# Performance work log

Hardware: AMD Instinct MI355X
Metric: run time of the kernel (lower is better)

## Reference

```python
import jax, jax.numpy as jnp
import numpy as np

EPS = 1e-5
NUM_GN_GROUPS = 32


def setup_inputs() -> dict:
    key = jax.random.key(0)
    k1, k2, k3 = jax.random.split(key, 3)
    B, C, N, G = 2, 256, 4096, 8
    c = C // G
    return {
        "points": jax.random.normal(k1, (B, C, N), dtype=jnp.float32),
        "conv_w": jax.random.normal(k2, (G, c, c), dtype=jnp.float32) / np.sqrt(c),
        "conv_b": jax.random.normal(k3, (C,), dtype=jnp.float32) * 0.02,
        "gn_w": jnp.ones((C,), dtype=jnp.float32),
        "gn_b": jnp.zeros((C,), dtype=jnp.float32),
    }


def reference(points, conv_w, conv_b, gn_w, gn_b):
    B, C, N = points.shape
    G = conv_w.shape[0]
    c = C // G  # channels per attention group
    identity = points

    # grouped 1x1 conv: per-group [c,c] matmul + bias
    x = points.reshape(B, G, c, N)
    x = jnp.einsum('gij,bgjn->bgin', conv_w, x) + conv_b.reshape(1, G, c, 1)

    # attention[b,g,n,m] = sum_i x[b,g,i,n] * x[b,g,i,m] / sqrt(c)
    scale = 1.0 / np.sqrt(c).astype(np.float32)
    attn = jnp.einsum('bgin,bgim->bgnm', x, x) * scale
    # softmax over dim=2 (the query/row N axis -- non-standard)
    attn = jax.nn.softmax(attn, axis=2)

    # ELU-gated second matmul: [B,G,c,N] @ [B,G,N,N] -> [B,G,c,N]
    x = jnp.einsum('bgcn,bgnm->bgcm', jax.nn.elu(x), attn)

    # channel shuffle: [B,G,c,N] -> [B,c,G,N] -> [B,C,N]
    x = x.transpose(0, 2, 1, 3).reshape(B, C, N)
    x = x + identity

    # GroupNorm(32 groups) over (channels-in-group, N)
    xg = x.reshape(B, NUM_GN_GROUPS, C // NUM_GN_GROUPS, N)
    mean = xg.mean(axis=(2, 3), keepdims=True)
    var = xg.var(axis=(2, 3), keepdims=True)
    xg = (xg - mean) * jax.lax.rsqrt(var + EPS)
    x = xg.reshape(B, C, N)
    return x * gn_w.reshape(1, C, 1) + gn_b.reshape(1, C, 1)
```

## Files before the change

kernel.cpp:

```cpp
#include <hip/hip_runtime.h>

typedef __attribute__((ext_vector_type(8))) short bf16x8;
typedef __attribute__((ext_vector_type(4))) short bf16x4;
typedef __attribute__((ext_vector_type(4))) float f32x4;

#if __has_builtin(__builtin_amdgcn_exp2f)
#define EXP2(x) __builtin_amdgcn_exp2f(x)
#else
#define EXP2(x) exp2f(x)
#endif

__device__ __forceinline__ unsigned short f2bf(float f) {
    union { float f; unsigned int u; } v; v.f = f;
    unsigned int r = v.u + 0x7fffu + ((v.u >> 16) & 1u);
    return (unsigned short)(r >> 16);
}

__device__ __forceinline__ float asf(unsigned int u) {
    union { unsigned int u; float f; } v; v.u = u; return v.f;
}

#define QK_PRESCALE 0.50500983f

__global__ __launch_bounds__(256) void conv_kernel(
    const float* __restrict__ points, const float* __restrict__ conv_w,
    const float* __restrict__ conv_b,
    unsigned short* __restrict__ xqT, unsigned short* __restrict__ xv)
{
    __shared__ float w[1024];
    const int h  = blockIdx.x >> 6;
    const int nc = blockIdx.x & 63;
    const int g  = h & 7;
    const int tid = threadIdx.x;
    const float* wg = conv_w + g * 1024;
    for (int k = tid; k < 1024; k += 256) w[k] = wg[k];
    __syncthreads();
    const int n  = nc * 64 + (tid & 63);
    const int ig = tid >> 6;
    const float* p = points + (size_t)h * 32 * 4096 + n;
    float pv[32];
#pragma unroll
    for (int j = 0; j < 32; ++j) pv[j] = p[(size_t)j * 4096];
    float out[8];
#pragma unroll
    for (int ii = 0; ii < 8; ++ii) {
        const int i = ig * 8 + ii;
        float acc = conv_b[g * 32 + i];
        const float4* w4 = (const float4*)(w + i * 32);
#pragma unroll
        for (int j4 = 0; j4 < 8; ++j4) {
            float4 ww = w4[j4];
            acc += ww.x * pv[j4 * 4]     + ww.y * pv[j4 * 4 + 1]
                 + ww.z * pv[j4 * 4 + 2] + ww.w * pv[j4 * 4 + 3];
        }
        out[ii] = acc;
    }
    unsigned short tq[8];
#pragma unroll
    for (int ii = 0; ii < 8; ++ii) tq[ii] = f2bf(out[ii] * QK_PRESCALE);
    *(bf16x8*)(xqT + ((size_t)h * 4096 + n) * 32 + ig * 8) = *(bf16x8*)tq;
#pragma unroll
    for (int ii = 0; ii < 8; ++ii) {
        float x = out[ii];
        float e = x > 0.f ? x : (__expf(x) - 1.f);
        xv[((size_t)h * 32 + ig * 8 + ii) * 4096 + n] = f2bf(e);
    }
}

#define VSTR 136
#define PSTR 72

#if __has_builtin(__builtin_amdgcn_cvt_pk_bf16_f32)
typedef __attribute__((ext_vector_type(2))) __bf16 bf16x2v;
__device__ __forceinline__ bf16x4 exp_pack(f32x4 sc, float& lsum) {
    float e0 = EXP2(sc[0]), e1 = EXP2(sc[1]);
    float e2 = EXP2(sc[2]), e3 = EXP2(sc[3]);
    lsum += (e0 + e1) + (e2 + e3);
    union { bf16x2v v[2]; bf16x4 s; } u;
    u.v[0] = __builtin_amdgcn_cvt_pk_bf16_f32(e0, e1);
    u.v[1] = __builtin_amdgcn_cvt_pk_bf16_f32(e2, e3);
    return u.s;
}
#else
__device__ __forceinline__ bf16x4 exp_pack(f32x4 sc, float& lsum) {
    union { float f; unsigned int u; } e0, e1, e2, e3;
    e0.f = EXP2(sc[0]); e1.f = EXP2(sc[1]); e2.f = EXP2(sc[2]); e3.f = EXP2(sc[3]);
    unsigned int t0 = e0.u & 0xffff0000u, t1 = e1.u & 0xffff0000u;
    unsigned int t2 = e2.u & 0xffff0000u, t3 = e3.u & 0xffff0000u;
    lsum += (asf(t0) + asf(t1)) + (asf(t2) + asf(t3));
    union { unsigned int d[2]; bf16x4 v; } pk;
    pk.d[0] = (t0 >> 16) | t1;
    pk.d[1] = (t2 >> 16) | t3;
    return pk.v;
}
#endif

#define CHUNK(C0, KU, KP, VCUR, VNXT)                                          \
    {                                                                          \
        __syncthreads();                                                       \
        *(bf16x8*)((VNXT) + vi * VSTR + vn)      = va;                         \
        *(bf16x8*)((VNXT) + vi * VSTR + vn + 64) = vb;                         \
        const int pf1 = ((C0) + 128) & 4095;                                   \
        const int pf2 = ((C0) + 256) & 4095;                                   \
        va = *(const bf16x8*)(vbase + (size_t)vi * 4096 + pf2 + vn);           \
        vb = *(const bf16x8*)(vbase + (size_t)vi * 4096 + pf2 + vn + 64);      \
        _Pragma("unroll")                                                      \
        for (int s8 = 0; s8 < 8; ++s8)                                         \
            KP[s8] = *(const bf16x8*)(kfp + (size_t)(pf1 + s8 * 16) * 32);     \
        _Pragma("unroll")                                                      \
        for (int sub = 0; sub < 2; ++sub) {                                    \
            _Pragma("unroll")                                                  \
            for (int s = 0; s < 4; ++s) {                                      \
                f32x4 sc = __builtin_amdgcn_mfma_f32_16x16x32_bf16(            \
                    KU[sub * 4 + s], qfrag, (f32x4){0.f, 0.f, 0.f, 0.f},       \
                    0, 0, 0);                                                  \
                bf16x4 pk = exp_pack(sc, lsum);                                \
                *(bf16x4*)(pw + l15 * PSTR + s * 16 + quad * 4) = pk;          \
            }                                                                  \
            _Pragma("unroll")                                                  \
            for (int ng = 0; ng < 2; ++ng) {                                   \
                bf16x8 pfrag = *(const bf16x8*)(pw + l15 * PSTR + ng * 32 +    \
                                                quad * 8);                     \
                const int col = sub * 64 + ng * 32 + quad * 8;                 \
                bf16x8 v0 = *(const bf16x8*)((VCUR) + l15 * VSTR + col);       \
                bf16x8 v1 = *(const bf16x8*)((VCUR) + (16 + l15) * VSTR + col);\
                acc0 = __builtin_amdgcn_mfma_f32_16x16x32_bf16(v0, pfrag,      \
                                                               acc0, 0, 0, 0); \
                acc1 = __builtin_amdgcn_mfma_f32_16x16x32_bf16(v1, pfrag,      \
                                                               acc1, 0, 0, 0); \
            }                                                                  \
        }                                                                      \
    }

__global__ __launch_bounds__(256, 4) void attn_kernel(
    const unsigned short* __restrict__ xqT,
    const unsigned short* __restrict__ xv,
    const float* __restrict__ points,
    float* __restrict__ z, float* __restrict__ pstats)
{
    __shared__ unsigned short Vt0[32 * VSTR];
    __shared__ unsigned short Vt1[32 * VSTR];
    __shared__ unsigned short Pl[4][16 * PSTR];

    const int bid = blockIdx.x;
    const int h  = (bid & 7) * 2 + ((bid >> 3) & 1);
    const int qt = bid >> 4;
    const int b = h >> 3, g = h & 7;
    const int tid = threadIdx.x;
    const int wv = tid >> 6, lane = tid & 63;
    const int quad = lane >> 4, l15 = lane & 15;

    const int m = qt * 64 + wv * 16 + l15;

    const unsigned short* kbase = xqT + (size_t)h * 4096 * 32;
    const unsigned short* vbase = xv  + (size_t)h * 32 * 4096;

    const bf16x8 qfrag = *(const bf16x8*)(kbase + (size_t)m * 32 + quad * 8);

    f32x4 acc0 = {0.f, 0.f, 0.f, 0.f};
    f32x4 acc1 = {0.f, 0.f, 0.f, 0.f};
    float lsum = 0.f;

    const int vi = tid >> 3, vn = (tid & 7) * 8;
    unsigned short* pw = &Pl[wv][0];

    const unsigned short* kfp = kbase + (size_t)l15 * 32 + quad * 8;

    {
        bf16x8 t0 = *(const bf16x8*)(vbase + (size_t)vi * 4096 + vn);
        bf16x8 t1 = *(const bf16x8*)(vbase + (size_t)vi * 4096 + vn + 64);
        *(bf16x8*)(Vt0 + vi * VSTR + vn)      = t0;
        *(bf16x8*)(Vt0 + vi * VSTR + vn + 64) = t1;
    }
    bf16x8 va = *(const bf16x8*)(vbase + (size_t)vi * 4096 + 128 + vn);
    bf16x8 vb = *(const bf16x8*)(vbase + (size_t)vi * 4096 + 128 + vn + 64);
    bf16x8 kA[8], kB[8];
#pragma unroll
    for (int s8 = 0; s8 < 8; ++s8)
        kA[s8] = *(const bf16x8*)(kfp + (size_t)(s8 * 16) * 32);

    for (int n0 = 0; n0 < 4096; n0 += 256) {
        CHUNK(n0,       kA, kB, Vt0, Vt1);
        CHUNK(n0 + 128, kB, kA, Vt1, Vt0);
    }

    lsum += __shfl_xor(lsum, 16, 64);
    lsum += __shfl_xor(lsum, 32, 64);
    const float inv = 1.f / lsum;

    const float* pb = points + (size_t)b * 256 * 4096;
    float* zb = z + (size_t)b * 256 * 4096;
    float* sb = pstats + ((size_t)bid * 4 + wv) * 64;

#pragma unroll
    for (int half = 0; half < 2; ++half) {
        f32x4 a = half ? acc1 : acc0;
#pragma unroll
        for (int r = 0; r < 4; ++r) {
            const int i = half * 16 + quad * 4 + r;
            const size_t off = (size_t)(i * 8 + g) * 4096;
            float zA = a[r] * inv + pb[off + m];
            zb[off + m] = zA;
            float s  = zA;
            float ss = zA * zA;
            s += __shfl_xor(s, 1, 64);  ss += __shfl_xor(ss, 1, 64);
            s += __shfl_xor(s, 2, 64);  ss += __shfl_xor(ss, 2, 64);
            s += __shfl_xor(s, 4, 64);  ss += __shfl_xor(ss, 4, 64);
            s += __shfl_xor(s, 8, 64);  ss += __shfl_xor(ss, 8, 64);
            if (l15 == 0) {
                sb[i * 2]     = s;
                sb[i * 2 + 1] = ss;
            }
        }
    }
}

__global__ __launch_bounds__(256) void gn_combine(const float* __restrict__ pstats,
                                                  float* __restrict__ stats)
{
    const int b = blockIdx.x >> 5;
    const int i = blockIdx.x & 31;
    const int tid = threadIdx.x;
    float s = 0.f, ss = 0.f;
    for (int k = tid; k < 2048; k += 256) {
        const int wvk = k & 3, j = k >> 2;
        const int bid = (j & 3) | (b << 2) | ((j >> 2) << 3);
        const float* p = pstats + ((size_t)bid * 4 + wvk) * 64 + i * 2;
        s += p[0]; ss += p[1];
    }
#pragma unroll
    for (int off = 32; off > 0; off >>= 1) {
        s  += __shfl_down(s, off, 64);
        ss += __shfl_down(ss, off, 64);
    }
    __shared__ float red[8];
    const int w = tid >> 6;
    if ((tid & 63) == 0) { red[w * 2] = s; red[w * 2 + 1] = ss; }
    __syncthreads();
    if (tid == 0) {
        s  = red[0] + red[2] + red[4] + red[6];
        ss = red[1] + red[3] + red[5] + red[7];
        float mean = s * (1.f / 32768.f);
        float var  = ss * (1.f / 32768.f) - mean * mean;
        stats[blockIdx.x * 2]     = mean;
        stats[blockIdx.x * 2 + 1] = rsqrtf(var + 1e-5f);
    }
}

__global__ __launch_bounds__(256) void gn_apply(float* __restrict__ z,
                                                const float* __restrict__ stats,
                                                const float* __restrict__ gw,
                                                const float* __restrict__ gb)
{
    const int idx = blockIdx.x * 256 + threadIdx.x;
    float4* p = (float4*)z;
    float4 v = p[idx];
    const int chg = idx >> 10;
    const int blk = chg >> 3;
    const int ch  = chg & 255;
    const float mean = stats[blk * 2], rstd = stats[blk * 2 + 1];
    const float w  = gw[ch] * rstd;
    const float bb = gb[ch] - mean * w;
    v.x = v.x * w + bb; v.y = v.y * w + bb;
    v.z = v.z * w + bb; v.w = v.w * w + bb;
    p[idx] = v;
}

extern "C" void kernel_launch(void* const* d_in, const int* in_sizes, int n_in,
                              void* d_out, int out_size, void* d_ws, size_t ws_size,
                              hipStream_t stream)
{
    const float* points = (const float*)d_in[0];
    const float* conv_w = (const float*)d_in[1];
    const float* conv_b = (const float*)d_in[2];
    const float* gn_w   = (const float*)d_in[3];
    const float* gn_b   = (const float*)d_in[4];
    float* out = (float*)d_out;
    char* ws = (char*)d_ws;
    unsigned short* xqT = (unsigned short*)ws;
    unsigned short* xv  = (unsigned short*)(ws + (size_t)4 * 1024 * 1024);
    float* pstats = (float*)(ws + (size_t)8 * 1024 * 1024);
    float* stats  = (float*)(ws + (size_t)9 * 1024 * 1024);

    conv_kernel<<<1024, 256, 0, stream>>>(points, conv_w, conv_b, xqT, xv);
    attn_kernel<<<1024, 256, 0, stream>>>(xqT, xv, points, out, pstats);
    gn_combine<<<64, 256, 0, stream>>>(pstats, stats);
    gn_apply<<<2048, 256, 0, stream>>>(out, stats, gn_w, gn_b);
}
```

Baseline: 158.0 us.

## Split attention key range in two halves with separate combine kernel

The attention kernel now splits the 4096-long key dimension into two halves, doubling the grid to 2048 blocks. Each block writes unnormalized partial outputs and partial softmax sums to workspace, and a new combine kernel merges them, adds the residual and emits GroupNorm partial stats. The V tile goes from double buffering to a single shared buffer with an extra barrier. This aims for more parallelism and occupancy, at the cost of partial-result traffic, an extra launch and more synchronization per chunk.

```diff
diff --git a/kernel.cpp b/kernel.cpp
--- a/kernel.cpp
+++ b/kernel.cpp
@@ -95,18 +95,18 @@
 }
 #endif
 
-#define CHUNK(C0, KU, KP, VCUR, VNXT)                                          \
+#define CHUNK(C0, KU, KP)                                                      \
     {                                                                          \
         __syncthreads();                                                       \
-        *(bf16x8*)((VNXT) + vi * VSTR + vn)      = va;                         \
-        *(bf16x8*)((VNXT) + vi * VSTR + vn + 64) = vb;                         \
-        const int pf1 = ((C0) + 128) & 4095;                                   \
-        const int pf2 = ((C0) + 256) & 4095;                                   \
-        va = *(const bf16x8*)(vbase + (size_t)vi * 4096 + pf2 + vn);           \
-        vb = *(const bf16x8*)(vbase + (size_t)vi * 4096 + pf2 + vn + 64);      \
+        *(bf16x8*)(Vt + vi * VSTR + vn)      = va;                             \
+        *(bf16x8*)(Vt + vi * VSTR + vn + 64) = vb;                             \
+        __syncthreads();                                                       \
+        const int pfb = ((C0) + 128) & 2047;                                   \
+        va = *(const bf16x8*)(vbaseh + (size_t)vi * 4096 + pfb + vn);          \
+        vb = *(const bf16x8*)(vbaseh + (size_t)vi * 4096 + pfb + vn + 64);     \
         _Pragma("unroll")                                                      \
         for (int s8 = 0; s8 < 8; ++s8)                                         \
-            KP[s8] = *(const bf16x8*)(kfp + (size_t)(pf1 + s8 * 16) * 32);     \
+            KP[s8] = *(const bf16x8*)(kfph + (size_t)(pfb + s8 * 16) * 32);    \
         _Pragma("unroll")                                                      \
         for (int sub = 0; sub < 2; ++sub) {                                    \
             _Pragma("unroll")                                                  \
@@ -122,8 +122,8 @@
                 bf16x8 pfrag = *(const bf16x8*)(pw + l15 * PSTR + ng * 32 +    \
                                                 quad * 8);                     \
                 const int col = sub * 64 + ng * 32 + quad * 8;                 \
-                bf16x8 v0 = *(const bf16x8*)((VCUR) + l15 * VSTR + col);       \
-                bf16x8 v1 = *(const bf16x8*)((VCUR) + (16 + l15) * VSTR + col);\
+                bf16x8 v0 = *(const bf16x8*)(Vt + l15 * VSTR + col);           \
+                bf16x8 v1 = *(const bf16x8*)(Vt + (16 + l15) * VSTR + col);    \
                 acc0 = __builtin_amdgcn_mfma_f32_16x16x32_bf16(v0, pfrag,      \
                                                                acc0, 0, 0, 0); \
                 acc1 = __builtin_amdgcn_mfma_f32_16x16x32_bf16(v1, pfrag,      \
@@ -135,17 +135,18 @@
 __global__ __launch_bounds__(256, 4) void attn_kernel(
     const unsigned short* __restrict__ xqT,
     const unsigned short* __restrict__ xv,
-    const float* __restrict__ points,
-    float* __restrict__ z, float* __restrict__ pstats)
-{
-    __shared__ unsigned short Vt0[32 * VSTR];
-    __shared__ unsigned short Vt1[32 * VSTR];
+    float* __restrict__ opart, float* __restrict__ lpart)
+{
+    __shared__ unsigned short Vt[32 * VSTR];
     __shared__ unsigned short Pl[4][16 * PSTR];
 
     const int bid = blockIdx.x;
-    const int h  = (bid & 7) * 2 + ((bid >> 3) & 1);
-    const int qt = bid >> 4;
-    const int b = h >> 3, g = h & 7;
+    const int x  = bid & 7;
+    const int r  = bid >> 3;
+    const int h  = x * 2 + (r & 1);
+    const int rr = r >> 1;
+    const int qt = rr & 63;
+    const int kh = rr >> 6;
     const int tid = threadIdx.x;
     const int wv = tid >> 6, lane = tid & 63;
     const int quad = lane >> 4, l15 = lane & 15;
@@ -153,7 +154,7 @@
     const int m = qt * 64 + wv * 16 + l15;
 
     const unsigned short* kbase = xqT + (size_t)h * 4096 * 32;
-    const unsigned short* vbase = xv  + (size_t)h * 32 * 4096;
+    const unsigned short* vbaseh = xv + (size_t)h * 32 * 4096 + kh * 2048;
 
     const bf16x8 qfrag = *(const bf16x8*)(kbase + (size_t)m * 32 + quad * 8);
 
@@ -164,54 +165,75 @@
     const int vi = tid >> 3, vn = (tid & 7) * 8;
     unsigned short* pw = &Pl[wv][0];
 
-    const unsigned short* kfp = kbase + (size_t)l15 * 32 + quad * 8;
-
-    {
-        bf16x8 t0 = *(const bf16x8*)(vbase + (size_t)vi * 4096 + vn);
-        bf16x8 t1 = *(const bf16x8*)(vbase + (size_t)vi * 4096 + vn + 64);
-        *(bf16x8*)(Vt0 + vi * VSTR + vn)      = t0;
-        *(bf16x8*)(Vt0 + vi * VSTR + vn + 64) = t1;
-    }
-    bf16x8 va = *(const bf16x8*)(vbase + (size_t)vi * 4096 + 128 + vn);
-    bf16x8 vb = *(const bf16x8*)(vbase + (size_t)vi * 4096 + 128 + vn + 64);
+    const unsigned short* kfph =
+        kbase + ((size_t)kh * 2048 + l15) * 32 + quad * 8;
+
+    bf16x8 va = *(const bf16x8*)(vbaseh + (size_t)vi * 4096 + vn);
+    bf16x8 vb = *(const bf16x8*)(vbaseh + (size_t)vi * 4096 + vn + 64);
     bf16x8 kA[8], kB[8];
 #pragma unroll
     for (int s8 = 0; s8 < 8; ++s8)
-        kA[s8] = *(const bf16x8*)(kfp + (size_t)(s8 * 16) * 32);
-
-    for (int n0 = 0; n0 < 4096; n0 += 256) {
-        CHUNK(n0,       kA, kB, Vt0, Vt1);
-        CHUNK(n0 + 128, kB, kA, Vt1, Vt0);
+        kA[s8] = *(const bf16x8*)(kfph + (size_t)(s8 * 16) * 32);
+
+    for (int n0 = 0; n0 < 2048; n0 += 256) {
+        CHUNK(n0,       kA, kB);
+        CHUNK(n0 + 128, kB, kA);
     }
 
     lsum += __shfl_xor(lsum, 16, 64);
     lsum += __shfl_xor(lsum, 32, 64);
-    const float inv = 1.f / lsum;
-
+
+    const int ml = wv * 16 + l15;
+    const size_t hq2 = ((size_t)h * 64 + qt) * 2 + kh;
+    float* ob = opart + hq2 * 2048;
+#pragma unroll
+    for (int half = 0; half < 2; ++half) {
+        f32x4 a = half ? acc1 : acc0;
+#pragma unroll
+        for (int rr2 = 0; rr2 < 4; ++rr2) {
+            const int i = half * 16 + quad * 4 + rr2;
+            ob[i * 64 + ml] = a[rr2];
+        }
+    }
+    if (quad == 0) lpart[hq2 * 64 + ml] = lsum;
+}
+
+__global__ __launch_bounds__(256) void combine_kernel(
+    const float* __restrict__ opart, const float* __restrict__ lpart,
+    const float* __restrict__ points, float* __restrict__ z,
+    float* __restrict__ pstats)
+{
+    const int bid2 = blockIdx.x;
+    const int h = bid2 >> 6, qt = bid2 & 63;
+    const int b = h >> 3, g = h & 7;
+    const int tid = threadIdx.x;
+    const int w = tid >> 6, lane = tid & 63;
+    const int mg = qt * 64 + lane;
+
+    const float la = lpart[(size_t)(bid2 * 2) * 64 + lane];
+    const float lb = lpart[(size_t)(bid2 * 2 + 1) * 64 + lane];
+    const float inv = 1.f / (la + lb);
+
+    const float* oa = opart + (size_t)(bid2 * 2) * 2048;
+    const float* obp = opart + (size_t)(bid2 * 2 + 1) * 2048;
     const float* pb = points + (size_t)b * 256 * 4096;
     float* zb = z + (size_t)b * 256 * 4096;
-    float* sb = pstats + ((size_t)bid * 4 + wv) * 64;
-
-#pragma unroll
-    for (int half = 0; half < 2; ++half) {
-        f32x4 a = half ? acc1 : acc0;
-#pragma unroll
-        for (int r = 0; r < 4; ++r) {
-            const int i = half * 16 + quad * 4 + r;
-            const size_t off = (size_t)(i * 8 + g) * 4096;
-            float zA = a[r] * inv + pb[off + m];
-            zb[off + m] = zA;
-            float s  = zA;
-            float ss = zA * zA;
-            s += __shfl_xor(s, 1, 64);  ss += __shfl_xor(ss, 1, 64);
-            s += __shfl_xor(s, 2, 64);  ss += __shfl_xor(ss, 2, 64);
-            s += __shfl_xor(s, 4, 64);  ss += __shfl_xor(ss, 4, 64);
-            s += __shfl_xor(s, 8, 64);  ss += __shfl_xor(ss, 8, 64);
-            if (l15 == 0) {
-                sb[i * 2]     = s;
-                sb[i * 2 + 1] = ss;
-            }
-        }
+    float* sb = pstats + (size_t)bid2 * 64;
+
+#pragma unroll
+    for (int ii = 0; ii < 8; ++ii) {
+        const int i = w * 8 + ii;
+        const size_t off = (size_t)(i * 8 + g) * 4096 + mg;
+        float v = (oa[i * 64 + lane] + obp[i * 64 + lane]) * inv + pb[off];
+        zb[off] = v;
+        float s = v, ss = v * v;
+        s += __shfl_xor(s, 1, 64);   ss += __shfl_xor(ss, 1, 64);
+        s += __shfl_xor(s, 2, 64);   ss += __shfl_xor(ss, 2, 64);
+        s += __shfl_xor(s, 4, 64);   ss += __shfl_xor(ss, 4, 64);
+        s += __shfl_xor(s, 8, 64);   ss += __shfl_xor(ss, 8, 64);
+        s += __shfl_xor(s, 16, 64);  ss += __shfl_xor(ss, 16, 64);
+        s += __shfl_xor(s, 32, 64);  ss += __shfl_xor(ss, 32, 64);
+        if (lane == 0) { sb[i * 2] = s; sb[i * 2 + 1] = ss; }
     }
 }
 
@@ -222,10 +244,8 @@
     const int i = blockIdx.x & 31;
     const int tid = threadIdx.x;
     float s = 0.f, ss = 0.f;
-    for (int k = tid; k < 2048; k += 256) {
-        const int wvk = k & 3, j = k >> 2;
-        const int bid = (j & 3) | (b << 2) | ((j >> 2) << 3);
-        const float* p = pstats + ((size_t)bid * 4 + wvk) * 64 + i * 2;
+    for (int k = tid; k < 512; k += 256) {
+        const float* p = pstats + (size_t)(b * 512 + k) * 64 + i * 2;
         s += p[0]; ss += p[1];
     }
 #pragma unroll
@@ -277,13 +297,17 @@
     const float* gn_b   = (const float*)d_in[4];
     float* out = (float*)d_out;
     char* ws = (char*)d_ws;
+    const size_t MB = 1024 * 1024;
     unsigned short* xqT = (unsigned short*)ws;
-    unsigned short* xv  = (unsigned short*)(ws + (size_t)4 * 1024 * 1024);
-    float* pstats = (float*)(ws + (size_t)8 * 1024 * 1024);
-    float* stats  = (float*)(ws + (size_t)9 * 1024 * 1024);
+    unsigned short* xv  = (unsigned short*)(ws + 4 * MB);
+    float* opart  = (float*)(ws + 8 * MB);
+    float* lpart  = (float*)(ws + 24 * MB);
+    float* pstats = (float*)(ws + 25 * MB);
+    float* stats  = (float*)(ws + 26 * MB);
 
     conv_kernel<<<1024, 256, 0, stream>>>(points, conv_w, conv_b, xqT, xv);
-    attn_kernel<<<1024, 256, 0, stream>>>(xqT, xv, points, out, pstats);
+    attn_kernel<<<2048, 256, 0, stream>>>(xqT, xv, opart, lpart);
+    combine_kernel<<<1024, 256, 0, stream>>>(opart, lpart, points, out, pstats);
     gn_combine<<<64, 256, 0, stream>>>(pstats, stats);
     gn_apply<<<2048, 256, 0, stream>>>(out, stats, gn_w, gn_b);
 }
```

After: 160.3 us. Within noise of the previous version (+1.5%).

## Load V fragments directly from global memory instead of LDS double-buffering

Applied to the files above, without the earlier changes.

The attention kernel no longer stages V tiles through shared memory with a per-chunk __syncthreads. Each wave now loads its own V MFMA operands straight from global/L2 into registers. This removes the block-wide barrier and LDS write/read traffic. In exchange, each of the four waves re-reads the same V data from cache, register pressure rises, and the launch-bounds occupancy hint drops from 4 to 3 blocks.

```diff
diff --git a/kernel.cpp b/kernel.cpp
--- a/kernel.cpp
+++ b/kernel.cpp
@@ -67,7 +67,6 @@
     }
 }
 
-#define VSTR 136
 #define PSTR 72
 
 #if __has_builtin(__builtin_amdgcn_cvt_pk_bf16_f32)
@@ -95,18 +94,18 @@
 }
 #endif
 
-#define CHUNK(C0, KU, KP, VCUR, VNXT)                                          \
+#define CHUNK(C0, KU, KP)                                                      \
     {                                                                          \
-        __syncthreads();                                                       \
-        *(bf16x8*)((VNXT) + vi * VSTR + vn)      = va;                         \
-        *(bf16x8*)((VNXT) + vi * VSTR + vn + 64) = vb;                         \
-        const int pf1 = ((C0) + 128) & 4095;                                   \
-        const int pf2 = ((C0) + 256) & 4095;                                   \
-        va = *(const bf16x8*)(vbase + (size_t)vi * 4096 + pf2 + vn);           \
-        vb = *(const bf16x8*)(vbase + (size_t)vi * 4096 + pf2 + vn + 64);      \
+        bf16x8 v[8];                                                           \
+        _Pragma("unroll")                                                      \
+        for (int q2 = 0; q2 < 4; ++q2) {                                       \
+            v[q2 * 2]     = *(const bf16x8*)(vp0 + (C0) + q2 * 32);            \
+            v[q2 * 2 + 1] = *(const bf16x8*)(vp1 + (C0) + q2 * 32);            \
+        }                                                                      \
+        const int pfb = ((C0) + 128) & 4095;                                   \
         _Pragma("unroll")                                                      \
         for (int s8 = 0; s8 < 8; ++s8)                                         \
-            KP[s8] = *(const bf16x8*)(kfp + (size_t)(pf1 + s8 * 16) * 32);     \
+            KP[s8] = *(const bf16x8*)(kfp + (size_t)(pfb + s8 * 16) * 32);     \
         _Pragma("unroll")                                                      \
         for (int sub = 0; sub < 2; ++sub) {                                    \
             _Pragma("unroll")                                                  \
@@ -121,30 +120,28 @@
             for (int ng = 0; ng < 2; ++ng) {                                   \
                 bf16x8 pfrag = *(const bf16x8*)(pw + l15 * PSTR + ng * 32 +    \
                                                 quad * 8);                     \
-                const int col = sub * 64 + ng * 32 + quad * 8;                 \
-                bf16x8 v0 = *(const bf16x8*)((VCUR) + l15 * VSTR + col);       \
-                bf16x8 v1 = *(const bf16x8*)((VCUR) + (16 + l15) * VSTR + col);\
-                acc0 = __builtin_amdgcn_mfma_f32_16x16x32_bf16(v0, pfrag,      \
-                                                               acc0, 0, 0, 0); \
-                acc1 = __builtin_amdgcn_mfma_f32_16x16x32_bf16(v1, pfrag,      \
-                                                               acc1, 0, 0, 0); \
+                const int q2 = sub * 2 + ng;                                   \
+                acc0 = __builtin_amdgcn_mfma_f32_16x16x32_bf16(                \
+                    v[q2 * 2], pfrag, acc0, 0, 0, 0);                          \
+                acc1 = __builtin_amdgcn_mfma_f32_16x16x32_bf16(                \
+                    v[q2 * 2 + 1], pfrag, acc1, 0, 0, 0);                      \
             }                                                                  \
         }                                                                      \
     }
 
-__global__ __launch_bounds__(256, 4) void attn_kernel(
+__global__ __launch_bounds__(256, 3) void attn_kernel(
     const unsigned short* __restrict__ xqT,
     const unsigned short* __restrict__ xv,
     const float* __restrict__ points,
     float* __restrict__ z, float* __restrict__ pstats)
 {
-    __shared__ unsigned short Vt0[32 * VSTR];
-    __shared__ unsigned short Vt1[32 * VSTR];
     __shared__ unsigned short Pl[4][16 * PSTR];
 
     const int bid = blockIdx.x;
-    const int h  = (bid & 7) * 2 + ((bid >> 3) & 1);
-    const int qt = bid >> 4;
+    const int x  = bid & 7;
+    const int r  = bid >> 3;
+    const int h  = x * 2 + (r & 1);
+    const int qt = r >> 1;
     const int b = h >> 3, g = h & 7;
     const int tid = threadIdx.x;
     const int wv = tid >> 6, lane = tid & 63;
@@ -161,27 +158,20 @@
     f32x4 acc1 = {0.f, 0.f, 0.f, 0.f};
     float lsum = 0.f;
 
-    const int vi = tid >> 3, vn = (tid & 7) * 8;
     unsigned short* pw = &Pl[wv][0];
 
     const unsigned short* kfp = kbase + (size_t)l15 * 32 + quad * 8;
-
-    {
-        bf16x8 t0 = *(const bf16x8*)(vbase + (size_t)vi * 4096 + vn);
-        bf16x8 t1 = *(const bf16x8*)(vbase + (size_t)vi * 4096 + vn + 64);
-        *(bf16x8*)(Vt0 + vi * VSTR + vn)      = t0;
-        *(bf16x8*)(Vt0 + vi * VSTR + vn + 64) = t1;
-    }
-    bf16x8 va = *(const bf16x8*)(vbase + (size_t)vi * 4096 + 128 + vn);
-    bf16x8 vb = *(const bf16x8*)(vbase + (size_t)vi * 4096 + 128 + vn + 64);
+    const unsigned short* vp0 = vbase + (size_t)l15 * 4096 + quad * 8;
+    const unsigned short* vp1 = vbase + (size_t)(16 + l15) * 4096 + quad * 8;
+
     bf16x8 kA[8], kB[8];
 #pragma unroll
     for (int s8 = 0; s8 < 8; ++s8)
         kA[s8] = *(const bf16x8*)(kfp + (size_t)(s8 * 16) * 32);
 
     for (int n0 = 0; n0 < 4096; n0 += 256) {
-        CHUNK(n0,       kA, kB, Vt0, Vt1);
-        CHUNK(n0 + 128, kB, kA, Vt1, Vt0);
+        CHUNK(n0,       kA, kB);
+        CHUNK(n0 + 128, kB, kA);
     }
 
     lsum += __shfl_xor(lsum, 16, 64);
@@ -196,10 +186,10 @@
     for (int half = 0; half < 2; ++half) {
         f32x4 a = half ? acc1 : acc0;
 #pragma unroll
-        for (int r = 0; r < 4; ++r) {
-            const int i = half * 16 + quad * 4 + r;
+        for (int rr = 0; rr < 4; ++rr) {
+            const int i = half * 16 + quad * 4 + rr;
             const size_t off = (size_t)(i * 8 + g) * 4096;
-            float zA = a[r] * inv + pb[off + m];
+            float zA = a[rr] * inv + pb[off + m];
             zb[off + m] = zA;
             float s  = zA;
             float ss = zA * zA;
@@ -277,10 +267,11 @@
     const float* gn_b   = (const float*)d_in[4];
     float* out = (float*)d_out;
     char* ws = (char*)d_ws;
+    const size_t MB = 1024 * 1024;
     unsigned short* xqT = (unsigned short*)ws;
-    unsigned short* xv  = (unsigned short*)(ws + (size_t)4 * 1024 * 1024);
-    float* pstats = (float*)(ws + (size_t)8 * 1024 * 1024);
-    float* stats  = (float*)(ws + (size_t)9 * 1024 * 1024);
+    unsigned short* xv  = (unsigned short*)(ws + 4 * MB);
+    float* pstats = (float*)(ws + 8 * MB);
+    float* stats  = (float*)(ws + 9 * MB);
 
     conv_kernel<<<1024, 256, 0, stream>>>(points, conv_w, conv_b, xqT, xv);
     attn_kernel<<<1024, 256, 0, stream>>>(xqT, xv, points, out, pstats);
```

Result: slower. 255.1 us (+61.5%).
